# Optimization experiments

Hardware: AMD Instinct MI355X
Metric: run time of the kernel (lower is better)

The kernel has to match this reference:

```python
import jax, jax.numpy as jnp
import numpy as np

B, N, D_IN, D, H, L, NQ, NC, HID = 4, 25000, 32, 256, 8, 6, 100, 18, 1024


def _ln(x, g, b, eps=1e-5):
    m = jnp.mean(x, -1, keepdims=True)
    v = jnp.mean((x - m) ** 2, -1, keepdims=True)
    return (x - m) / jnp.sqrt(v + eps) * g + b


def _mha(q, kv, wqkv, bqkv, wo, bo, h):
    # q: (B, Lq, d), kv: (B, Lk, d); torch nn.MultiheadAttention math
    d = q.shape[-1]
    dh = d // h
    wq, wk, wv = jnp.split(wqkv, 3, axis=0)
    bq, bk, bv = jnp.split(bqkv, 3)
    Q = (q @ wq.T + bq).reshape(q.shape[0], q.shape[1], h, dh)
    K = (kv @ wk.T + bk).reshape(kv.shape[0], kv.shape[1], h, dh)
    V = (kv @ wv.T + bv).reshape(kv.shape[0], kv.shape[1], h, dh)
    s = jnp.einsum('bqhd,bkhd->bhqk', Q, K) / jnp.asarray(np.sqrt(dh), Q.dtype)
    a = jax.nn.softmax(s, axis=-1)
    o = jnp.einsum('bhqk,bkhd->bqhd', a, V).reshape(q.shape)
    return o @ wo.T + bo


def setup_inputs() -> dict:
    key = jax.random.key(0)
    ks = list(jax.random.split(key, 20))
    ki = iter(ks)

    def p(shape, s=0.02):
        return jax.random.normal(next(ki), shape, jnp.float32) * s

    inp = {
        'x': jax.random.normal(next(ki), (B * N, D_IN), jnp.float32),
        'batch_offsets': jnp.arange(B + 1, dtype=jnp.int32) * N,
        'ip_w': p((D, D_IN)), 'ip_b': jnp.zeros((D,), jnp.float32),
        'ip_ln_g': jnp.ones((D,), jnp.float32), 'ip_ln_b': jnp.zeros((D,), jnp.float32),
        'xm_w1': p((D, D_IN)), 'xm_b1': jnp.zeros((D,), jnp.float32),
        'xm_w2': p((D, D)), 'xm_b2': jnp.zeros((D,), jnp.float32),
        'query_embed': p((NQ, D), 1.0),
        'ca_wqkv': p((L, 3 * D, D)), 'ca_bqkv': jnp.zeros((L, 3 * D), jnp.float32),
        'ca_wo': p((L, D, D)), 'ca_bo': jnp.zeros((L, D), jnp.float32),
        'sa_wqkv': p((L, 3 * D, D)), 'sa_bqkv': jnp.zeros((L, 3 * D), jnp.float32),
        'sa_wo': p((L, D, D)), 'sa_bo': jnp.zeros((L, D), jnp.float32),
        'sa_ln_g': jnp.ones((L, D), jnp.float32), 'sa_ln_b': jnp.zeros((L, D), jnp.float32),
        'ffn_w1': p((L, HID, D)), 'ffn_b1': jnp.zeros((L, HID), jnp.float32),
        'ffn_w2': p((L, D, HID)), 'ffn_b2': jnp.zeros((L, D), jnp.float32),
        'ffn_ln_g': jnp.ones((L, D), jnp.float32), 'ffn_ln_b': jnp.zeros((L, D), jnp.float32),
        'out_ln_g': jnp.ones((D,), jnp.float32), 'out_ln_b': jnp.zeros((D,), jnp.float32),
        'cls_w1': p((D, D)), 'cls_b1': jnp.zeros((D,), jnp.float32),
        'cls_w2': p((NC + 1, D)), 'cls_b2': jnp.zeros((NC + 1,), jnp.float32),
    }
    return inp


def reference(x, batch_offsets, ip_w, ip_b, ip_ln_g, ip_ln_b, xm_w1, xm_b1, xm_w2, xm_b2,
              query_embed, ca_wqkv, ca_bqkv, ca_wo, ca_bo, sa_wqkv, sa_bqkv, sa_wo, sa_bo,
              sa_ln_g, sa_ln_b, ffn_w1, ffn_b1, ffn_w2, ffn_b2, ffn_ln_g, ffn_ln_b,
              out_ln_g, out_ln_b, cls_w1, cls_b1, cls_w2, cls_b2):
    b = batch_offsets.shape[0] - 1  # uniform segments -> batched attention
    n = x.shape[0] // b
    # input_proj: Linear -> LayerNorm -> ReLU
    inst = jax.nn.relu(_ln(x @ ip_w.T + ip_b, ip_ln_g, ip_ln_b)).reshape(b, n, -1)
    # x_mask: Linear -> ReLU -> Linear
    mask_feats = (jax.nn.relu(x @ xm_w1.T + xm_b1) @ xm_w2.T + xm_b2).reshape(b, n, -1)
    query = jnp.broadcast_to(query_embed, (b,) + query_embed.shape)
    for i in range(ca_wqkv.shape[0]):
        # CrossAttentionLayer: NOTE original discards dropout/norm results -> pure residual
        query = _mha(query, inst, ca_wqkv[i], ca_bqkv[i], ca_wo[i], ca_bo[i], H) + query
        # SelfAttentionLayer: residual + LayerNorm
        query = _ln(_mha(query, query, sa_wqkv[i], sa_bqkv[i], sa_wo[i], sa_bo[i], H) + query,
                    sa_ln_g[i], sa_ln_b[i])
        # FFN: residual + LayerNorm
        ff = jax.nn.relu(query @ ffn_w1[i].T + ffn_b1[i]) @ ffn_w2[i].T + ffn_b2[i]
        query = _ln(ff + query, ffn_ln_g[i], ffn_ln_b[i])
    qn = _ln(query, out_ln_g, out_ln_b)
    pred_labels = jax.nn.relu(qn @ cls_w1.T + cls_b1) @ cls_w2.T + cls_b2  # (b, NQ, NC+1)
    pred_masks = jnp.einsum('bqd,bnd->bqn', qn, mask_feats)  # (b, NQ, n)
    return pred_labels, pred_masks
```

## Files before the change

### kernel.cpp

```cpp
#include <hip/hip_runtime.h>

typedef unsigned short u16;
typedef unsigned int   u32;

constexpr int Bz   = 4;
constexpr int Ni   = 25000;
constexpr int BNi  = Bz * Ni;
constexpr int DIN  = 32;
constexpr int D    = 256;
constexpr int Hh   = 8;
constexpr int DH   = 32;
constexpr int Ll   = 6;
constexpr int NQ   = 100;
constexpr int NC1  = 19;
constexpr int HIDd = 1024;

constexpr int CHUNK  = 1250;
constexpr int NCHUNK = Ni / CHUNK;
constexpr size_t PARTB = (size_t)Hh * NCHUNK * 128 * 34;
constexpr float SM_SCALE = 0.17677669529663687f;

__device__ __forceinline__ u16 f2b(float f) {
    union { __bf16 h; u16 u; } c; c.h = (__bf16)f; return c.u;
}
__device__ __forceinline__ u32 pk2(float a, float b) {
    union { __bf16 h[2]; u32 u; } c; c.h[0] = (__bf16)a; c.h[1] = (__bf16)b; return c.u;
}

__global__ void k_cvt(const float* __restrict__ in, u16* __restrict__ out, int n) {
    for (int i = blockIdx.x * blockDim.x + threadIdx.x; i < n; i += gridDim.x * blockDim.x)
        out[i] = f2b(in[i]);
}

struct CvtJobs { const float* s[9]; u16* d[9]; int n[9]; };
__global__ __launch_bounds__(256) void k_cvtall(CvtJobs j) {
    const int job = blockIdx.y;
    const float* s = j.s[job];
    u16* d = j.d[job];
    const int n = j.n[job];
    for (int i = blockIdx.x * 256 + threadIdx.x; i < n; i += gridDim.x * 256)
        d[i] = f2b(s[i]);
}

__device__ __forceinline__ void gload16(const u16* g, u16* l) {
    __builtin_amdgcn_global_load_lds(
        (const __attribute__((address_space(1))) void*)g,
        (__attribute__((address_space(3))) void*)l, 16, 0, 0);
}

typedef __attribute__((ext_vector_type(8))) __bf16 bf8v;
typedef __attribute__((ext_vector_type(8))) short  s8v;
typedef __attribute__((ext_vector_type(4))) float  f4v;

template<bool DOLN>
__global__ __launch_bounds__(512) void k_inproj(
    const float* __restrict__ x, int row0, int Mloc,
    const u16* __restrict__ w16, const float* __restrict__ bias,
    const float* __restrict__ g, const float* __restrict__ bb,
    u16* __restrict__ outb)
{
    __shared__ u16 Ws[256 * 40];
    __shared__ float Cb[256], Cg[256], Cbb[256];
    const int tid = threadIdx.x, lane = tid & 63, w = tid >> 6;
    const int lr = lane & 15, hi = lane >> 4;

    for (int ch = tid; ch < 1024; ch += 512) {
        int r = ch >> 2, g4 = ch & 3;
        *(uint4*)&Ws[r * 40 + g4 * 8] = *(const uint4*)(w16 + r * 32 + g4 * 8);
    }
    if (tid < 256) {
        Cb[tid] = bias[tid];
        if (DOLN) { Cg[tid] = g[tid]; Cbb[tid] = bb[tid]; }
    }

    const int rloc = blockIdx.x * 128 + w * 16 + lr;
    const int gr = row0 + min(rloc, Mloc - 1);
    bf8v xf;
    {
        const float* xp = x + (size_t)gr * DIN + hi * 8;
        float4 a = *(const float4*)xp, c = *(const float4*)(xp + 4);
        union { s8v s; bf8v b; } u;
        u.s[0] = (short)f2b(a.x); u.s[1] = (short)f2b(a.y);
        u.s[2] = (short)f2b(a.z); u.s[3] = (short)f2b(a.w);
        u.s[4] = (short)f2b(c.x); u.s[5] = (short)f2b(c.y);
        u.s[6] = (short)f2b(c.z); u.s[7] = (short)f2b(c.w);
        xf = u.b;
    }
    __syncthreads();

    f4v acc[16];
    #pragma unroll
    for (int ci = 0; ci < 16; ci++) {
        acc[ci] = (f4v){0.f, 0.f, 0.f, 0.f};
        bf8v af = *(const bf8v*)&Ws[(ci * 16 + lr) * 40 + hi * 8];
        acc[ci] = __builtin_amdgcn_mfma_f32_16x16x32_bf16(af, xf, acc[ci], 0, 0, 0);
    }
    #pragma unroll
    for (int ci = 0; ci < 16; ci++)
        #pragma unroll
        for (int r = 0; r < 4; r++)
            acc[ci][r] += Cb[ci * 16 + hi * 4 + r];

    float mean = 0.f, ri = 1.f;
    if (DOLN) {
        float s = 0.f, q = 0.f;
        #pragma unroll
        for (int ci = 0; ci < 16; ci++)
            #pragma unroll
            for (int r = 0; r < 4; r++) { s += acc[ci][r]; q += acc[ci][r] * acc[ci][r]; }
        s += __shfl_xor(s, 16); s += __shfl_xor(s, 32);
        q += __shfl_xor(q, 16); q += __shfl_xor(q, 32);
        mean = s * (1.f / D);
        float var = q * (1.f / D) - mean * mean;
        ri = rsqrtf(var + 1e-5f);
    }
    if (rloc < Mloc) {
        #pragma unroll
        for (int ci = 0; ci < 16; ci++) {
            float v0[4];
            #pragma unroll
            for (int r = 0; r < 4; r++) {
                float v = acc[ci][r];
                if (DOLN) v = (v - mean) * ri * Cg[ci * 16 + hi * 4 + r] + Cbb[ci * 16 + hi * 4 + r];
                v0[r] = fmaxf(v, 0.f);
            }
            uint2 pkv;
            pkv.x = pk2(v0[0], v0[1]);
            pkv.y = pk2(v0[2], v0[3]);
            *(uint2*)&outb[(size_t)rloc * 256 + ci * 16 + hi * 4] = pkv;
        }
    }
}

__global__ __launch_bounds__(256) void k_ln(
    const float* __restrict__ in, float* __restrict__ out,
    const float* __restrict__ g, const float* __restrict__ b)
{
    const int t = threadIdx.x;
    const int row = blockIdx.x;
    float v = in[(size_t)row * D + t];
    float s = v, q = v * v;
    #pragma unroll
    for (int off = 32; off >= 1; off >>= 1) { s += __shfl_xor(s, off); q += __shfl_xor(q, off); }
    __shared__ float red[2][4];
    const int wid = t >> 6;
    if ((t & 63) == 0) { red[0][wid] = s; red[1][wid] = q; }
    __syncthreads();
    float S = red[0][0] + red[0][1] + red[0][2] + red[0][3];
    float Q = red[1][0] + red[1][1] + red[1][2] + red[1][3];
    float m   = S * (1.f / D);
    float var = Q * (1.f / D) - m * m;
    float ri  = rsqrtf(var + 1e-5f);
    out[(size_t)row * D + t] = (v - m) * ri * g[t] + b[t];
}

__global__ __launch_bounds__(256) void k_bcast(const float* __restrict__ qe, float* __restrict__ q)
{
    const int t = threadIdx.x;
    const int r = blockIdx.x;
    q[(size_t)r * D + t] = qe[(size_t)(r % NQ) * D + t];
}

template<int BM, int BN, int TM, int TN>
__global__ __launch_bounds__(256) void k_gemm(
    const float* __restrict__ A, const float* __restrict__ W,
    const float* __restrict__ bias, const float* __restrict__ resid,
    float* __restrict__ C, int M, int N, int K, int relu)
{
    constexpr int BK = 16;
    constexpr int TX = BN / TN, TY = BM / TM;
    static_assert(TX * TY == 256, "block must be 256 threads");
    __shared__ float As[BK][BM + 4];
    __shared__ float Ws[BK][BN + 4];

    const int tid = threadIdx.x;
    const int tx = tid % TX, ty = tid / TX;
    const int row0 = blockIdx.y * BM, col0 = blockIdx.x * BN;

    float acc[TM][TN];
    #pragma unroll
    for (int i = 0; i < TM; i++)
        #pragma unroll
        for (int j = 0; j < TN; j++) acc[i][j] = 0.f;

    for (int k0 = 0; k0 < K; k0 += BK) {
        __syncthreads();
        for (int idx = tid; idx < BM * (BK / 4); idx += 256) {
            int r = idx / (BK / 4), c4 = idx % (BK / 4);
            int gr = row0 + r;
            float4 v;
            if (gr < M) v = *(const float4*)(A + (size_t)gr * K + k0 + c4 * 4);
            else { v.x = v.y = v.z = v.w = 0.f; }
            As[c4*4+0][r] = v.x; As[c4*4+1][r] = v.y; As[c4*4+2][r] = v.z; As[c4*4+3][r] = v.w;
        }
        for (int idx = tid; idx < BN * (BK / 4); idx += 256) {
            int n = idx / (BK / 4), c4 = idx % (BK / 4);
            int gn = col0 + n;
            float4 v;
            if (gn < N) v = *(const float4*)(W + (size_t)gn * K + k0 + c4 * 4);
            else { v.x = v.y = v.z = v.w = 0.f; }
            Ws[c4*4+0][n] = v.x; Ws[c4*4+1][n] = v.y; Ws[c4*4+2][n] = v.z; Ws[c4*4+3][n] = v.w;
        }
        __syncthreads();
        #pragma unroll
        for (int kk = 0; kk < BK; kk++) {
            float a[TM], bb[TN];
            #pragma unroll
            for (int i = 0; i < TM; i++) a[i] = As[kk][ty * TM + i];
            #pragma unroll
            for (int j = 0; j < TN; j++) bb[j] = Ws[kk][tx * TN + j];
            #pragma unroll
            for (int i = 0; i < TM; i++)
                #pragma unroll
                for (int j = 0; j < TN; j++)
                    acc[i][j] = fmaf(a[i], bb[j], acc[i][j]);
        }
    }

    #pragma unroll
    for (int i = 0; i < TM; i++) {
        int gr = row0 + ty * TM + i;
        if (gr >= M) continue;
        #pragma unroll
        for (int j = 0; j < TN; j++) {
            int gn = col0 + tx * TN + j;
            if (gn >= N) continue;
            float v = acc[i][j];
            if (bias)  v += bias[gn];
            if (resid) v += resid[(size_t)gr * N + gn];
            if (relu)  v = fmaxf(v, 0.f);
            C[(size_t)gr * N + gn] = v;
        }
    }
}

template<bool RELU>
__global__ __launch_bounds__(256) void mm_small(
    const float* __restrict__ A, const u16* __restrict__ W,
    const float* __restrict__ bias, const float* __restrict__ resid,
    float* __restrict__ C, int M, int N, int K)
{
    __shared__ u16 As[64 * 40];
    __shared__ u16 Bs[64 * 40];
    const int tid  = threadIdx.x;
    const int lane = tid & 63, w = tid >> 6;
    const int wm = w >> 1, wn = w & 1;
    const int row0 = blockIdx.y * 64, col0 = blockIdx.x * 64;
    const int lr = lane & 15, hi = lane >> 4;

    f4v acc[2][2];
    #pragma unroll
    for (int i = 0; i < 2; i++)
        #pragma unroll
        for (int j = 0; j < 2; j++) acc[i][j] = (f4v){0.f, 0.f, 0.f, 0.f};

    const int sr = tid >> 2, sc = (tid & 3) * 8;
    const int ga = min(row0 + sr, M - 1);
    const int gw = min(col0 + sr, N - 1);

    for (int k0 = 0; k0 < K; k0 += 32) {
        __syncthreads();
        {
            const float* ap = A + (size_t)ga * K + k0 + sc;
            float4 a = *(const float4*)ap, c = *(const float4*)(ap + 4);
            uint4 u;
            u.x = pk2(a.x, a.y); u.y = pk2(a.z, a.w);
            u.z = pk2(c.x, c.y); u.w = pk2(c.z, c.w);
            *(uint4*)&As[sr * 40 + sc] = u;
            *(uint4*)&Bs[sr * 40 + sc] = *(const uint4*)(W + (size_t)gw * K + k0 + sc);
        }
        __syncthreads();
        bf8v a0 = *(const bf8v*)&As[(wm * 32      + lr) * 40 + hi * 8];
        bf8v a1 = *(const bf8v*)&As[(wm * 32 + 16 + lr) * 40 + hi * 8];
        bf8v b0 = *(const bf8v*)&Bs[(wn * 32      + lr) * 40 + hi * 8];
        bf8v b1 = *(const bf8v*)&Bs[(wn * 32 + 16 + lr) * 40 + hi * 8];
        acc[0][0] = __builtin_amdgcn_mfma_f32_16x16x32_bf16(a0, b0, acc[0][0], 0, 0, 0);
        acc[0][1] = __builtin_amdgcn_mfma_f32_16x16x32_bf16(a0, b1, acc[0][1], 0, 0, 0);
        acc[1][0] = __builtin_amdgcn_mfma_f32_16x16x32_bf16(a1, b0, acc[1][0], 0, 0, 0);
        acc[1][1] = __builtin_amdgcn_mfma_f32_16x16x32_bf16(a1, b1, acc[1][1], 0, 0, 0);
    }

    const int crl = hi * 4, ccl = lr;
    #pragma unroll
    for (int mi = 0; mi < 2; mi++)
        #pragma unroll
        for (int ni = 0; ni < 2; ni++)
            #pragma unroll
            for (int r = 0; r < 4; r++) {
                int grow = row0 + wm * 32 + mi * 16 + crl + r;
                int gcol = col0 + wn * 32 + ni * 16 + ccl;
                if (grow < M && gcol < N) {
                    float v = acc[mi][ni][r];
                    if (bias)  v += bias[gcol];
                    if (resid) v += resid[(size_t)grow * N + gcol];
                    if (RELU)  v = fmaxf(v, 0.f);
                    C[(size_t)grow * N + gcol] = v;
                }
            }
}

template<bool OUTBF>
__global__ __launch_bounds__(256) void mm128(
    const u16* __restrict__ A, const u16* __restrict__ W,
    const float* __restrict__ bias, void* __restrict__ Cv,
    int M, int N, int K, long long sA, long long sW, long long sC,
    int zmod, long long sW2, long long sBias)
{
    __shared__ u16 sm[8192];
    u16* As = sm;
    u16* Bs = sm + 4096;

    const int gx = gridDim.x, gy = gridDim.y;
    const int total = gx * gy * (int)gridDim.z;
    const int flat = blockIdx.x + gx * (blockIdx.y + gy * blockIdx.z);
    const int q8 = total >> 3, r8 = total & 7;
    const int xcd = flat & 7, blk = flat >> 3;
    const int swz = (xcd < r8 ? xcd * (q8 + 1) : r8 * (q8 + 1) + (xcd - r8) * q8) + blk;
    const int bx = swz % gx, by = (swz / gx) % gy, bz = swz / (gx * gy);

    const int aidx = bz % zmod, widx = bz / zmod;
    A += (size_t)aidx * sA;
    W += (size_t)aidx * sW + (size_t)widx * sW2;
    if (bias) bias += (size_t)widx * sBias;
    const int tid = threadIdx.x, lane = tid & 63, w = tid >> 6;
    const int wm = w >> 1, wn = w & 1;
    const int row0 = by * 128, col0 = bx * 128;
    const int lr = lane & 15, hi = lane >> 4;
    const int srow = lane >> 2, scol = (lane & 3) * 8;

    f4v acc[4][4];
    #pragma unroll
    for (int i = 0; i < 4; i++)
        #pragma unroll
        for (int j = 0; j < 4; j++) acc[i][j] = (f4v){0.f, 0.f, 0.f, 0.f};

    for (int k0 = 0; k0 < K; k0 += 32) {
        __syncthreads();
        #pragma unroll
        for (int i = 0; i < 2; i++) {
            const int c = w * 2 + i;
            const int row = c * 16 + srow;
            const int gra = min(row0 + row, M - 1);
            const int grb = min(col0 + row, N - 1);
            gload16(A + (size_t)gra * K + k0 + scol, &As[c * 512]);
            gload16(W + (size_t)grb * K + k0 + scol, &Bs[c * 512]);
        }
        __syncthreads();
        bf8v a[4], bb[4];
        #pragma unroll
        for (int mi = 0; mi < 4; mi++)
            a[mi] = *(const bf8v*)&As[(wm * 64 + mi * 16 + lr) * 32 + hi * 8];
        #pragma unroll
        for (int ni = 0; ni < 4; ni++)
            bb[ni] = *(const bf8v*)&Bs[(wn * 64 + ni * 16 + lr) * 32 + hi * 8];
        #pragma unroll
        for (int mi = 0; mi < 4; mi++)
            #pragma unroll
            for (int ni = 0; ni < 4; ni++)
                acc[mi][ni] = __builtin_amdgcn_mfma_f32_16x16x32_bf16(a[mi], bb[ni], acc[mi][ni], 0, 0, 0);
    }

    if (OUTBF) {
        #pragma unroll
        for (int h0 = 0; h0 < 2; h0++) {
            __syncthreads();
            if (wm == h0) {
                #pragma unroll
                for (int mi = 0; mi < 4; mi++)
                    #pragma unroll
                    for (int ni = 0; ni < 4; ni++) {
                        int gcol = col0 + wn * 64 + ni * 16 + lr;
                        float bv = bias ? bias[gcol] : 0.f;
                        #pragma unroll
                        for (int r = 0; r < 4; r++) {
                            int lrow = mi * 16 + hi * 4 + r;
                            sm[lrow * 128 + wn * 64 + ni * 16 + lr] = f2b(acc[mi][ni][r] + bv);
                        }
                    }
            }
            __syncthreads();
            u16* Cb16 = (u16*)Cv + (size_t)bz * sC;
            #pragma unroll
            for (int j = 0; j < 4; j++) {
                int idx = tid + j * 256;
                int lrow = idx >> 4, c16 = idx & 15;
                int grow = row0 + h0 * 64 + lrow;
                if (grow < M)
                    *(uint4*)(Cb16 + (size_t)grow * N + col0 + c16 * 8) =
                        *(const uint4*)&sm[lrow * 128 + c16 * 8];
            }
        }
    } else {
        const int crl = hi * 4, ccl = lr;
        float* Cf = (float*)Cv + (size_t)bz * sC;
        #pragma unroll
        for (int mi = 0; mi < 4; mi++)
            #pragma unroll
            for (int ni = 0; ni < 4; ni++)
                #pragma unroll
                for (int r = 0; r < 4; r++) {
                    int grow = row0 + wm * 64 + mi * 16 + crl + r;
                    int gcol = col0 + wn * 64 + ni * 16 + ccl;
                    if (grow < M && gcol < N) {
                        float v = acc[mi][ni][r];
                        if (bias) v += bias[gcol];
                        Cf[(size_t)grow * N + gcol] = v;
                    }
                }
    }
}

__global__ __launch_bounds__(512) void k_flash(
    const float* __restrict__ qbuf, const u16* __restrict__ kv,
    float* __restrict__ part, int bBase, size_t kvStride, size_t pStride)
{
    const int tid = threadIdx.x;
    const int lane = tid & 63, w = tid >> 6;
    const int h = blockIdx.y;
    const int b = bBase + blockIdx.z;
    const u16* kvp = kv + (size_t)blockIdx.z * kvStride;
    float* pp = part + (size_t)blockIdx.z * pStride;
    const int k0loc = blockIdx.x * CHUNK;
    const int lr = lane & 15, hi = lane >> 4;

    __shared__ u16 Ks[64 * 40];
    __shared__ u16 Vt[32 * 72];
    __shared__ u16 Pt[8][16 * 72];

    const int qt = w * 16 + lr;
    const int qg = b * NQ + min(qt, NQ - 1);
    bf8v qf;
    {
        const float* Qp = qbuf + (size_t)qg * D + h * DH + hi * 8;
        union { s8v s; bf8v b; } qu;
        #pragma unroll
        for (int j = 0; j < 8; j++) qu.s[j] = (short)f2b(Qp[j] * SM_SCALE);
        qf = qu.b;
    }

    float m = -1e30f, l = 0.f;
    f4v o0 = (f4v){0.f,0.f,0.f,0.f}, o1 = (f4v){0.f,0.f,0.f,0.f};

    constexpr int NSTEP = (CHUNK + 63) / 64;
    for (int s = 0; s < NSTEP; s++) {
        const int ck = k0loc + s * 64;
        const int nv = min(64, k0loc + CHUNK - ck);
        __syncthreads();
        if (tid < 256) {
            int key = tid >> 2, g = tid & 3;
            int krow = min(ck + key, Ni - 1);
            *(uint4*)&Ks[key * 40 + g * 8] =
                *(const uint4*)(kvp + (size_t)krow * (2 * D) + h * DH + g * 8);
        } else {
            int t2 = tid - 256;
            int key = t2 >> 2, g = t2 & 3;
            int krow = min(ck + key, Ni - 1);
            uint4 u = *(const uint4*)(kvp + (size_t)krow * (2 * D) + D + h * DH + g * 8);
            const u16* pu = (const u16*)&u;
            #pragma unroll
            for (int j = 0; j < 8; j++) Vt[(g * 8 + j) * 72 + key] = pu[j];
        }
        __syncthreads();

        f4v sf[4];
        #pragma unroll
        for (int j = 0; j < 4; j++) {
            bf8v kf = *(const bf8v*)&Ks[(j * 16 + lr) * 40 + hi * 8];
            sf[j] = (f4v){0.f,0.f,0.f,0.f};
            sf[j] = __builtin_amdgcn_mfma_f32_16x16x32_bf16(kf, qf, sf[j], 0, 0, 0);
        }

        float sv[16];
        #pragma unroll
        for (int j = 0; j < 4; j++)
            #pragma unroll
            for (int r = 0; r < 4; r++) {
                int key0 = j * 16 + hi * 4 + r;
                sv[j * 4 + r] = (key0 < nv) ? sf[j][r] : -1e30f;
            }
        float smax = sv[0];
        #pragma unroll
        for (int j = 1; j < 16; j++) smax = fmaxf(smax, sv[j]);
        smax = fmaxf(smax, __shfl_xor(smax, 16));
        smax = fmaxf(smax, __shfl_xor(smax, 32));
        float mnew  = fmaxf(m, smax);
        float scale = __expf(m - mnew);
        m = mnew;

        float pv[16];
        float psum = 0.f;
        #pragma unroll
        for (int j = 0; j < 16; j++) {
            pv[j] = __expf(sv[j] - mnew);
            psum += pv[j];
        }
        psum += __shfl_xor(psum, 16);
        psum += __shfl_xor(psum, 32);
        l = l * scale + psum;

        u16* pw = &Pt[w][lr * 72];
        #pragma unroll
        for (int j = 0; j < 4; j++) {
            *(u32*)&pw[j * 16 + hi * 4]     = pk2(pv[j*4+0], pv[j*4+1]);
            *(u32*)&pw[j * 16 + hi * 4 + 2] = pk2(pv[j*4+2], pv[j*4+3]);
        }

        const int qb4 = hi * 4;
        float f0 = __shfl(scale, qb4 + 0);
        float f1 = __shfl(scale, qb4 + 1);
        float f2 = __shfl(scale, qb4 + 2);
        float f3 = __shfl(scale, qb4 + 3);
        o0[0] *= f0; o0[1] *= f1; o0[2] *= f2; o0[3] *= f3;
        o1[0] *= f0; o1[1] *= f1; o1[2] *= f2; o1[3] *= f3;

        #pragma unroll
        for (int j = 0; j < 2; j++) {
            bf8v pf  = *(const bf8v*)&Pt[w][lr * 72 + j * 32 + hi * 8];
            bf8v vf0 = *(const bf8v*)&Vt[lr * 72 + j * 32 + hi * 8];
            bf8v vf1 = *(const bf8v*)&Vt[(16 + lr) * 72 + j * 32 + hi * 8];
            o0 = __builtin_amdgcn_mfma_f32_16x16x32_bf16(pf, vf0, o0, 0, 0, 0);
            o1 = __builtin_amdgcn_mfma_f32_16x16x32_bf16(pf, vf1, o1, 0, 0, 0);
        }
    }

    const size_t pbase = ((size_t)(h * NCHUNK + blockIdx.x) * 128) * 34;
    #pragma unroll
    for (int r = 0; r < 4; r++) {
        int qtr = w * 16 + hi * 4 + r;
        pp[pbase + (size_t)qtr * 34 + 2 + lr]      = o0[r];
        pp[pbase + (size_t)qtr * 34 + 2 + 16 + lr] = o1[r];
    }
    if (lane < 16) {
        pp[pbase + (size_t)(w * 16 + lane) * 34 + 0] = m;
        pp[pbase + (size_t)(w * 16 + lane) * 34 + 1] = l;
    }
}

__global__ __launch_bounds__(64) void k_fmerge(const float* __restrict__ part,
                                               float* __restrict__ abuf, int bBase, size_t pStride)
{
    const float* pz = part + (size_t)blockIdx.y * pStride;
    const int b = bBase + blockIdx.y;
    const int t = threadIdx.x;
    const int hq = blockIdx.x;
    const int h = hq / NQ, q = hq % NQ;
    float mmax = -1e30f;
    for (int c = 0; c < NCHUNK; c++)
        mmax = fmaxf(mmax, pz[((size_t)(h * NCHUNK + c) * 128 + q) * 34]);
    float L = 0.f, a = 0.f;
    for (int c = 0; c < NCHUNK; c++) {
        const float* p = &pz[((size_t)(h * NCHUNK + c) * 128 + q) * 34];
        float wv = __expf(p[0] - mmax);
        L += wv * p[1];
        if (t < DH) a += wv * p[2 + t];
    }
    if (t < DH)
        abuf[((size_t)(b * NQ + q)) * D + h * DH + t] = a / L;
}

__global__ __launch_bounds__(128) void k_sattn(const float* __restrict__ sqkv, float* __restrict__ abuf)
{
    const int tid = threadIdx.x;
    const int bh = blockIdx.x;
    const int b = bh >> 3, h = bh & 7;
    __shared__ float Ks[NQ][DH], Vs[NQ][DH];
    for (int idx = tid; idx < NQ * 8; idx += 128) {
        int kk = idx >> 3, f4 = idx & 7;
        const float* base = sqkv + ((size_t)(b * NQ + kk)) * (3 * D) + h * DH;
        *(float4*)&Ks[kk][f4 * 4] = *(const float4*)(base + D + f4 * 4);
        *(float4*)&Vs[kk][f4 * 4] = *(const float4*)(base + 2 * D + f4 * 4);
    }
    float qr[DH];
    const int q = tid;
    if (q < NQ) {
        const float* Qp = sqkv + ((size_t)(b * NQ + q)) * (3 * D) + h * DH;
        #pragma unroll
        for (int d = 0; d < DH; d += 4) {
            float4 v = *(const float4*)(Qp + d);
            qr[d] = v.x * SM_SCALE; qr[d+1] = v.y * SM_SCALE;
            qr[d+2] = v.z * SM_SCALE; qr[d+3] = v.w * SM_SCALE;
        }
    } else {
        #pragma unroll
        for (int d = 0; d < DH; d++) qr[d] = 0.f;
    }
    __syncthreads();
    float m = -1e30f, l = 0.f, acc[DH];
    #pragma unroll
    for (int d = 0; d < DH; d++) acc[d] = 0.f;
    for (int kk = 0; kk < NQ; kk++) {
        float sc = 0.f;
        #pragma unroll
        for (int d = 0; d < DH; d++) sc += qr[d] * Ks[kk][d];
        if (sc > m) {
            float r = __expf(m - sc);
            l *= r;
            #pragma unroll
            for (int d = 0; d < DH; d++) acc[d] *= r;
            m = sc;
        }
        float p = __expf(sc - m);
        l += p;
        #pragma unroll
        for (int d = 0; d < DH; d++) acc[d] += p * Vs[kk][d];
    }
    if (q < NQ) {
        float li = 1.f / l;
        float* o = abuf + ((size_t)(b * NQ + q)) * D + h * DH;
        #pragma unroll
        for (int d = 0; d < DH; d++) o[d] = acc[d] * li;
    }
}

extern "C" void kernel_launch(void* const* d_in, const int* in_sizes, int n_in,
                              void* d_out, int out_size, void* d_ws, size_t ws_size,
                              hipStream_t stream)
{
    const float* x        = (const float*)d_in[0];
    const float* ip_w     = (const float*)d_in[2];
    const float* ip_b     = (const float*)d_in[3];
    const float* ip_g     = (const float*)d_in[4];
    const float* ip_bb    = (const float*)d_in[5];
    const float* xm_w1    = (const float*)d_in[6];
    const float* xm_b1    = (const float*)d_in[7];
    const float* xm_w2    = (const float*)d_in[8];
    const float* xm_b2    = (const float*)d_in[9];
    const float* qe       = (const float*)d_in[10];
    const float* ca_wqkv  = (const float*)d_in[11];
    const float* ca_bqkv  = (const float*)d_in[12];
    const float* ca_wo    = (const float*)d_in[13];
    const float* ca_bo    = (const float*)d_in[14];
    const float* sa_wqkv  = (const float*)d_in[15];
    const float* sa_bqkv  = (const float*)d_in[16];
    const float* sa_wo    = (const float*)d_in[17];
    const float* sa_bo    = (const float*)d_in[18];
    const float* sa_ln_g  = (const float*)d_in[19];
    const float* sa_ln_b  = (const float*)d_in[20];
    const float* ffn_w1   = (const float*)d_in[21];
    const float* ffn_b1   = (const float*)d_in[22];
    const float* ffn_w2   = (const float*)d_in[23];
    const float* ffn_b2   = (const float*)d_in[24];
    const float* ffn_ln_g = (const float*)d_in[25];
    const float* ffn_ln_b = (const float*)d_in[26];
    const float* out_ln_g = (const float*)d_in[27];
    const float* out_ln_b = (const float*)d_in[28];
    const float* cls_w1   = (const float*)d_in[29];
    const float* cls_b1   = (const float*)d_in[30];
    const float* cls_w2   = (const float*)d_in[31];
    const float* cls_b2   = (const float*)d_in[32];
    float* out = (float*)d_out;

    bool batched = false;
    int kvG = 1;
    int instRows;
    if      (ws_size >= 740000000ull) { batched = true; kvG = 6; instRows = BNi; }
    else if (ws_size >= 430000000ull) { batched = true; kvG = 3; instRows = BNi; }
    else if (ws_size >= 210000000ull) { batched = true; kvG = 1; instRows = BNi; }
    else if (ws_size >= 112000000ull) { instRows = BNi; }
    else if (ws_size >=  73000000ull) { instRows = Ni;  }
    else return;
    const bool instFull = (instRows == BNi);
    const int nzb = batched ? Bz : 1;

    char* wp = (char*)d_ws;
    auto alloc = [&](size_t bytes) -> char* {
        char* r = wp; wp += (bytes + 255) & ~(size_t)255; return r;
    };
    u16*   instb = (u16*)  alloc((size_t)instRows * D * 2);
    u16*   kvb   = (u16*)  alloc((batched ? (size_t)kvG * Bz * Ni * 2 * D : (size_t)Ni * 2 * D) * 2);
    float* part  = (float*)alloc((size_t)nzb * PARTB * 4);
    float* qbuf  = (float*)alloc(409600);
    float* abuf  = (float*)alloc(409600);
    float* sqkv  = (float*)alloc(1228800);
    float* f1b   = (float*)alloc(1638400);
    float* qA    = (float*)alloc(409600);
    float* qB    = (float*)alloc(409600);
    u16*   ipw16 = (u16*)  alloc(256 * 32 * 2);
    u16*   xw116 = (u16*)  alloc(256 * 32 * 2);
    u16*   xw216 = (u16*)  alloc((size_t)D * D * 2);
    u16*   caq16 = (u16*)  alloc((size_t)Ll * 3 * D * D * 2);
    u16*   saq16 = (u16*)  alloc((size_t)Ll * 3 * D * D * 2);
    u16*   cao16 = (u16*)  alloc((size_t)Ll * D * D * 2);
    u16*   sao16 = (u16*)  alloc((size_t)Ll * D * D * 2);
    u16*   fw116 = (u16*)  alloc((size_t)Ll * HIDd * D * 2);
    u16*   fw216 = (u16*)  alloc((size_t)Ll * D * HIDd * 2);
    u16*   qnb   = (u16*)  alloc((size_t)Bz * NQ * D * 2);

    {
        CvtJobs j;
        j.s[0] = ip_w;    j.d[0] = ipw16; j.n[0] = 256 * 32;
        j.s[1] = xm_w1;   j.d[1] = xw116; j.n[1] = 256 * 32;
        j.s[2] = xm_w2;   j.d[2] = xw216; j.n[2] = D * D;
        j.s[3] = ca_wqkv; j.d[3] = caq16; j.n[3] = Ll * 3 * D * D;
        j.s[4] = sa_wqkv; j.d[4] = saq16; j.n[4] = Ll * 3 * D * D;
        j.s[5] = ca_wo;   j.d[5] = cao16; j.n[5] = Ll * D * D;
        j.s[6] = sa_wo;   j.d[6] = sao16; j.n[6] = Ll * D * D;
        j.s[7] = ffn_w1;  j.d[7] = fw116; j.n[7] = Ll * HIDd * D;
        j.s[8] = ffn_w2;  j.d[8] = fw216; j.n[8] = Ll * D * HIDd;
        k_cvtall<<<dim3(48, 9), 256, 0, stream>>>(j);
    }

    if (instFull)
        k_inproj<true><<<(BNi + 127) / 128, 512, 0, stream>>>(
            x, 0, BNi, ipw16, ip_b, ip_g, ip_bb, instb);
    k_bcast<<<Bz * NQ, 256, 0, stream>>>(qe, qA);

    float* qcur = qA;
    float* qtmp = qB;

    auto layer_tail = [&](int i) {
        mm_small<false><<<dim3(4, 7), 256, 0, stream>>>(
            abuf, cao16 + (size_t)i * D * D, ca_bo + (size_t)i * D, qcur, qtmp,
            Bz * NQ, D, D);
        { float* t2 = qcur; qcur = qtmp; qtmp = t2; }
        mm_small<false><<<dim3(12, 7), 256, 0, stream>>>(
            qcur, saq16 + (size_t)i * 3 * D * D, sa_bqkv + (size_t)i * 3 * D, nullptr, sqkv,
            Bz * NQ, 3 * D, D);
        k_sattn<<<Bz * Hh, 128, 0, stream>>>(sqkv, abuf);
        mm_small<false><<<dim3(4, 7), 256, 0, stream>>>(
            abuf, sao16 + (size_t)i * D * D, sa_bo + (size_t)i * D, qcur, qtmp,
            Bz * NQ, D, D);
        k_ln<<<Bz * NQ, 256, 0, stream>>>(qtmp, qtmp, sa_ln_g + i * D, sa_ln_b + i * D);
        { float* t2 = qcur; qcur = qtmp; qtmp = t2; }
        mm_small<true><<<dim3(16, 7), 256, 0, stream>>>(
            qcur, fw116 + (size_t)i * HIDd * D, ffn_b1 + (size_t)i * HIDd, nullptr, f1b,
            Bz * NQ, HIDd, D);
        mm_small<false><<<dim3(4, 7), 256, 0, stream>>>(
            f1b, fw216 + (size_t)i * D * HIDd, ffn_b2 + (size_t)i * D, qcur, qtmp,
            Bz * NQ, D, HIDd);
        k_ln<<<Bz * NQ, 256, 0, stream>>>(qtmp, qtmp, ffn_ln_g + i * D, ffn_ln_b + i * D);
        { float* t2 = qcur; qcur = qtmp; qtmp = t2; }
    };

    if (batched) {
        for (int l0 = 0; l0 < Ll; l0 += kvG) {
            mm128<true><<<dim3(4, 196, 4 * kvG), 256, 0, stream>>>(
                instb, caq16 + (size_t)l0 * 3 * D * D + (size_t)D * D,
                ca_bqkv + (size_t)l0 * 3 * D + D, kvb, Ni, 2 * D, D,
                (long long)Ni * D, 0, (long long)Ni * 2 * D,
                4, (long long)3 * D * D, (long long)3 * D);
            for (int i = l0; i < l0 + kvG; i++) {
                const u16* wq16 = caq16 + (size_t)i * 3 * D * D;
                const float* bqkv = ca_bqkv + (size_t)i * 3 * D;
                mm_small<false><<<dim3(4, 7), 256, 0, stream>>>(
                    qcur, wq16, bqkv, nullptr, qbuf, Bz * NQ, D, D);
                const u16* kvl = kvb + (size_t)(i - l0) * Bz * Ni * 2 * D;
                k_flash<<<dim3(NCHUNK, Hh, 4), 512, 0, stream>>>(
                    qbuf, kvl, part, 0, (size_t)Ni * 2 * D, PARTB);
                k_fmerge<<<dim3(Hh * NQ, 4), 64, 0, stream>>>(part, abuf, 0, PARTB);
                layer_tail(i);
            }
        }
    } else {
        for (int i = 0; i < Ll; i++) {
            const u16* wq16  = caq16 + (size_t)i * 3 * D * D;
            const u16* wkv16 = wq16 + (size_t)D * D;
            const float* bqkv = ca_bqkv + (size_t)i * 3 * D;
            mm_small<false><<<dim3(4, 7), 256, 0, stream>>>(
                qcur, wq16, bqkv, nullptr, qbuf, Bz * NQ, D, D);
            for (int b = 0; b < Bz; b++) {
                if (!instFull)
                    k_inproj<true><<<(Ni + 127) / 128, 512, 0, stream>>>(
                        x, b * Ni, Ni, ipw16, ip_b, ip_g, ip_bb, instb);
                const u16* ip = instFull ? instb + (size_t)b * Ni * D : instb;
                mm128<true><<<dim3(4, 196, 1), 256, 0, stream>>>(
                    ip, wkv16, bqkv + D, kvb, Ni, 2 * D, D, 0, 0, 0, 4, 0, 0);
                k_flash<<<dim3(NCHUNK, Hh, 1), 512, 0, stream>>>(
                    qbuf, kvb, part, b, 0, 0);
                k_fmerge<<<dim3(Hh * NQ, 1), 64, 0, stream>>>(part, abuf, b, 0);
            }
            layer_tail(i);
        }
    }

    float* qn = qbuf;
    k_ln<<<Bz * NQ, 256, 0, stream>>>(qcur, qn, out_ln_g, out_ln_b);
    k_gemm<64,64,4,4><<<dim3(4, 7), 256, 0, stream>>>(
        qn, cls_w1, cls_b1, nullptr, abuf, Bz * NQ, D, D, 1);
    k_gemm<64,64,4,4><<<dim3(1, 7), 256, 0, stream>>>(
        abuf, cls_w2, cls_b2, nullptr, out, Bz * NQ, NC1, D, 0);

    k_cvt<<<128, 256, 0, stream>>>(qn, qnb, Bz * NQ * D);
    if (instFull) {
        k_inproj<false><<<(BNi + 127) / 128, 512, 0, stream>>>(
            x, 0, BNi, xw116, xm_b1, nullptr, nullptr, instb);
        if (batched) {
            mm128<true><<<dim3(2, 196, 4), 256, 0, stream>>>(
                instb, xw216, xm_b2, kvb, Ni, D, D,
                (long long)Ni * D, 0, (long long)Ni * D, 4, 0, 0);
            mm128<false><<<dim3(196, 1, 4), 256, 0, stream>>>(
                qnb, kvb, nullptr, out + Bz * NQ * NC1, NQ, Ni, D,
                (long long)NQ * D, (long long)Ni * D, (long long)NQ * Ni, 4, 0, 0);
        } else {
            for (int b = 0; b < Bz; b++) {
                mm128<true><<<dim3(2, 196, 1), 256, 0, stream>>>(
                    instb + (size_t)b * Ni * D, xw216, xm_b2, kvb, Ni, D, D, 0, 0, 0, 4, 0, 0);
                mm128<false><<<dim3(196, 1, 1), 256, 0, stream>>>(
                    qnb + (size_t)b * NQ * D, kvb, nullptr,
                    out + Bz * NQ * NC1 + (size_t)b * NQ * Ni, NQ, Ni, D, 0, 0, 0, 4, 0, 0);
            }
        }
    } else {
        for (int b = 0; b < Bz; b++) {
            k_inproj<false><<<(Ni + 127) / 128, 512, 0, stream>>>(
                x, b * Ni, Ni, xw116, xm_b1, nullptr, nullptr, instb);
            mm128<true><<<dim3(2, 196, 1), 256, 0, stream>>>(
                instb, xw216, xm_b2, kvb, Ni, D, D, 0, 0, 0, 4, 0, 0);
            mm128<false><<<dim3(196, 1, 1), 256, 0, stream>>>(
                qnb + (size_t)b * NQ * D, kvb, nullptr,
                out + Bz * NQ * NC1 + (size_t)b * NQ * Ni, NQ, Ni, D, 0, 0, 0, 4, 0, 0);
        }
    }
}
```

Measured before the change: 1.710 ms.

## Fuse cross-attention K/V projection into flash attention kernel

The separate K/V projection GEMM, which wrote a large bf16 KV buffer, is removed. Each flash-attention block now loads its head's K and V weight slices into shared memory and computes the K/V tiles for 32 keys at a time from the inst activations. The block index is remapped so neighbouring blocks, likely sharing an XCD, work on the same batch and chunk. This cuts HBM traffic for the KV write and read but recomputes the projection per head, halves the key step, and drops the workspace-size fallback paths.

Result: slower. 1.960 ms (+14.6%).

```diff
diff --git a/kernel.cpp b/kernel.cpp
--- a/kernel.cpp
+++ b/kernel.cpp
@@ -17,6 +17,8 @@
 
 constexpr int CHUNK  = 1250;
 constexpr int NCHUNK = Ni / CHUNK;
+constexpr int KSTEP  = 32;
+constexpr int NSTEP  = (CHUNK + KSTEP - 1) / KSTEP;
 constexpr size_t PARTB = (size_t)Hh * NCHUNK * 128 * 34;
 constexpr float SM_SCALE = 0.17677669529663687f;
 
@@ -410,69 +412,110 @@
     }
 }
 
-__global__ __launch_bounds__(512) void k_flash(
-    const float* __restrict__ qbuf, const u16* __restrict__ kv,
-    float* __restrict__ part, int bBase, size_t kvStride, size_t pStride)
-{
-    const int tid = threadIdx.x;
-    const int lane = tid & 63, w = tid >> 6;
-    const int h = blockIdx.y;
-    const int b = bBase + blockIdx.z;
-    const u16* kvp = kv + (size_t)blockIdx.z * kvStride;
-    float* pp = part + (size_t)blockIdx.z * pStride;
-    const int k0loc = blockIdx.x * CHUNK;
+__global__ __launch_bounds__(512) void k_fused(
+    const float* __restrict__ qbuf, const u16* __restrict__ instb,
+    const u16* __restrict__ wk,
+    const float* __restrict__ bkv,
+    float* __restrict__ part)
+{
+    __shared__ u16 Wks[32 * 264];
+    __shared__ u16 Wvs[32 * 264];
+    __shared__ u16 instT[32 * 264];
+    __shared__ u16 Ks[32 * 40];
+    __shared__ u16 Vt[32 * 40];
+    u16* Pt = instT;
+
+    const int f = blockIdx.x + NCHUNK * (blockIdx.y + Hh * (int)blockIdx.z);
+    const int xcd = f & 7, slot = f >> 3;
+    const int g = xcd * 10 + (slot >> 3);
+    const int h = slot & 7;
+    const int c = g % NCHUNK, b = g / NCHUNK;
+
+    const int tid = threadIdx.x, lane = tid & 63, w = tid >> 6;
     const int lr = lane & 15, hi = lane >> 4;
-
-    __shared__ u16 Ks[64 * 40];
-    __shared__ u16 Vt[32 * 72];
-    __shared__ u16 Pt[8][16 * 72];
+    const int k0loc = c * CHUNK;
+    const u16* instB = instb + (size_t)b * Ni * D;
+    const u16* wkh = wk + (size_t)(h * DH) * D;
+    const u16* wvh = wk + (size_t)D * D + (size_t)(h * DH) * D;
+
+    for (int idx = tid; idx < 2048; idx += 512) {
+        int which = idx >> 10;
+        int r = (idx >> 5) & 31, c8 = idx & 31;
+        const u16* src = (which ? wvh : wkh) + (size_t)r * D + c8 * 8;
+        u16* dst = (which ? Wvs : Wks) + r * 264 + c8 * 8;
+        *(uint4*)dst = *(const uint4*)src;
+    }
 
     const int qt = w * 16 + lr;
     const int qg = b * NQ + min(qt, NQ - 1);
     bf8v qf;
     {
         const float* Qp = qbuf + (size_t)qg * D + h * DH + hi * 8;
-        union { s8v s; bf8v b; } qu;
+        union { s8v s; bf8v b2; } qu;
         #pragma unroll
         for (int j = 0; j < 8; j++) qu.s[j] = (short)f2b(Qp[j] * SM_SCALE);
-        qf = qu.b;
+        qf = qu.b2;
+    }
+
+    const int isV = w >> 2;
+    const int w2 = w & 3;
+    const int ktw = w2 & 1, dtw = w2 >> 1;
+    float kb = 0.f, vb[4];
+    if (!isV) {
+        kb = bkv[h * DH + dtw * 16 + lr];
+    } else {
+        #pragma unroll
+        for (int r = 0; r < 4; r++) vb[r] = bkv[D + h * DH + dtw * 16 + hi * 4 + r];
     }
 
     float m = -1e30f, l = 0.f;
     f4v o0 = (f4v){0.f,0.f,0.f,0.f}, o1 = (f4v){0.f,0.f,0.f,0.f};
 
-    constexpr int NSTEP = (CHUNK + 63) / 64;
     for (int s = 0; s < NSTEP; s++) {
-        const int ck = k0loc + s * 64;
-        const int nv = min(64, k0loc + CHUNK - ck);
-        __syncthreads();
-        if (tid < 256) {
-            int key = tid >> 2, g = tid & 3;
-            int krow = min(ck + key, Ni - 1);
-            *(uint4*)&Ks[key * 40 + g * 8] =
-                *(const uint4*)(kvp + (size_t)krow * (2 * D) + h * DH + g * 8);
+        const int ck = k0loc + s * KSTEP;
+        const int nv = min(KSTEP, k0loc + CHUNK - ck);
+        __syncthreads();
+        for (int idx = tid; idx < 1024; idx += 512) {
+            int r = idx >> 5, c8 = idx & 31;
+            int grow = min(ck + r, Ni - 1);
+            *(uint4*)&instT[r * 264 + c8 * 8] =
+                *(const uint4*)(instB + (size_t)grow * D + c8 * 8);
+        }
+        __syncthreads();
+        f4v pacc = (f4v){0.f,0.f,0.f,0.f};
+        #pragma unroll
+        for (int kk = 0; kk < 8; kk++) {
+            bf8v af, bf;
+            if (!isV) {
+                af = *(const bf8v*)&instT[(ktw * 16 + lr) * 264 + kk * 32 + hi * 8];
+                bf = *(const bf8v*)&Wks[(dtw * 16 + lr) * 264 + kk * 32 + hi * 8];
+            } else {
+                af = *(const bf8v*)&Wvs[(dtw * 16 + lr) * 264 + kk * 32 + hi * 8];
+                bf = *(const bf8v*)&instT[(ktw * 16 + lr) * 264 + kk * 32 + hi * 8];
+            }
+            pacc = __builtin_amdgcn_mfma_f32_16x16x32_bf16(af, bf, pacc, 0, 0, 0);
+        }
+        if (!isV) {
+            #pragma unroll
+            for (int r = 0; r < 4; r++)
+                Ks[(ktw * 16 + hi * 4 + r) * 40 + dtw * 16 + lr] = f2b(pacc[r] + kb);
         } else {
-            int t2 = tid - 256;
-            int key = t2 >> 2, g = t2 & 3;
-            int krow = min(ck + key, Ni - 1);
-            uint4 u = *(const uint4*)(kvp + (size_t)krow * (2 * D) + D + h * DH + g * 8);
-            const u16* pu = (const u16*)&u;
-            #pragma unroll
-            for (int j = 0; j < 8; j++) Vt[(g * 8 + j) * 72 + key] = pu[j];
-        }
-        __syncthreads();
-
-        f4v sf[4];
-        #pragma unroll
-        for (int j = 0; j < 4; j++) {
+            #pragma unroll
+            for (int r = 0; r < 4; r++)
+                Vt[(dtw * 16 + hi * 4 + r) * 40 + ktw * 16 + lr] = f2b(pacc[r] + vb[r]);
+        }
+        __syncthreads();
+
+        f4v sf[2];
+        #pragma unroll
+        for (int j = 0; j < 2; j++) {
             bf8v kf = *(const bf8v*)&Ks[(j * 16 + lr) * 40 + hi * 8];
             sf[j] = (f4v){0.f,0.f,0.f,0.f};
             sf[j] = __builtin_amdgcn_mfma_f32_16x16x32_bf16(kf, qf, sf[j], 0, 0, 0);
         }
-
-        float sv[16];
-        #pragma unroll
-        for (int j = 0; j < 4; j++)
+        float sv[8];
+        #pragma unroll
+        for (int j = 0; j < 2; j++)
             #pragma unroll
             for (int r = 0; r < 4; r++) {
                 int key0 = j * 16 + hi * 4 + r;
@@ -480,27 +523,24 @@
             }
         float smax = sv[0];
         #pragma unroll
-        for (int j = 1; j < 16; j++) smax = fmaxf(smax, sv[j]);
+        for (int j = 1; j < 8; j++) smax = fmaxf(smax, sv[j]);
         smax = fmaxf(smax, __shfl_xor(smax, 16));
         smax = fmaxf(smax, __shfl_xor(smax, 32));
         float mnew  = fmaxf(m, smax);
         float scale = __expf(m - mnew);
         m = mnew;
 
-        float pv[16];
+        float pv[8];
         float psum = 0.f;
         #pragma unroll
-        for (int j = 0; j < 16; j++) {
-            pv[j] = __expf(sv[j] - mnew);
-            psum += pv[j];
-        }
+        for (int j = 0; j < 8; j++) { pv[j] = __expf(sv[j] - mnew); psum += pv[j]; }
         psum += __shfl_xor(psum, 16);
         psum += __shfl_xor(psum, 32);
         l = l * scale + psum;
 
-        u16* pw = &Pt[w][lr * 72];
-        #pragma unroll
-        for (int j = 0; j < 4; j++) {
+        u16* pw = &Pt[(size_t)w * 640 + lr * 40];
+        #pragma unroll
+        for (int j = 0; j < 2; j++) {
             *(u32*)&pw[j * 16 + hi * 4]     = pk2(pv[j*4+0], pv[j*4+1]);
             *(u32*)&pw[j * 16 + hi * 4 + 2] = pk2(pv[j*4+2], pv[j*4+3]);
         }
@@ -513,17 +553,15 @@
         o0[0] *= f0; o0[1] *= f1; o0[2] *= f2; o0[3] *= f3;
         o1[0] *= f0; o1[1] *= f1; o1[2] *= f2; o1[3] *= f3;
 
-        #pragma unroll
-        for (int j = 0; j < 2; j++) {
-            bf8v pf  = *(const bf8v*)&Pt[w][lr * 72 + j * 32 + hi * 8];
-            bf8v vf0 = *(const bf8v*)&Vt[lr * 72 + j * 32 + hi * 8];
-            bf8v vf1 = *(const bf8v*)&Vt[(16 + lr) * 72 + j * 32 + hi * 8];
-            o0 = __builtin_amdgcn_mfma_f32_16x16x32_bf16(pf, vf0, o0, 0, 0, 0);
-            o1 = __builtin_amdgcn_mfma_f32_16x16x32_bf16(pf, vf1, o1, 0, 0, 0);
-        }
-    }
-
-    const size_t pbase = ((size_t)(h * NCHUNK + blockIdx.x) * 128) * 34;
+        bf8v pf  = *(const bf8v*)&Pt[(size_t)w * 640 + lr * 40 + hi * 8];
+        bf8v vf0 = *(const bf8v*)&Vt[lr * 40 + hi * 8];
+        bf8v vf1 = *(const bf8v*)&Vt[(16 + lr) * 40 + hi * 8];
+        o0 = __builtin_amdgcn_mfma_f32_16x16x32_bf16(pf, vf0, o0, 0, 0, 0);
+        o1 = __builtin_amdgcn_mfma_f32_16x16x32_bf16(pf, vf1, o1, 0, 0, 0);
+    }
+
+    float* pp = part + (size_t)b * PARTB;
+    const size_t pbase = ((size_t)(h * NCHUNK + c) * 128) * 34;
     #pragma unroll
     for (int r = 0; r < 4; r++) {
         int qtr = w * 16 + hi * 4 + r;
@@ -650,25 +688,15 @@
     const float* cls_b2   = (const float*)d_in[32];
     float* out = (float*)d_out;
 
-    bool batched = false;
-    int kvG = 1;
-    int instRows;
-    if      (ws_size >= 740000000ull) { batched = true; kvG = 6; instRows = BNi; }
-    else if (ws_size >= 430000000ull) { batched = true; kvG = 3; instRows = BNi; }
-    else if (ws_size >= 210000000ull) { batched = true; kvG = 1; instRows = BNi; }
-    else if (ws_size >= 112000000ull) { instRows = BNi; }
-    else if (ws_size >=  73000000ull) { instRows = Ni;  }
-    else return;
-    const bool instFull = (instRows == BNi);
-    const int nzb = batched ? Bz : 1;
+    if (ws_size < 160000000ull) return;
 
     char* wp = (char*)d_ws;
     auto alloc = [&](size_t bytes) -> char* {
         char* r = wp; wp += (bytes + 255) & ~(size_t)255; return r;
     };
-    u16*   instb = (u16*)  alloc((size_t)instRows * D * 2);
-    u16*   kvb   = (u16*)  alloc((batched ? (size_t)kvG * Bz * Ni * 2 * D : (size_t)Ni * 2 * D) * 2);
-    float* part  = (float*)alloc((size_t)nzb * PARTB * 4);
+    u16*   instb = (u16*)  alloc((size_t)BNi * D * 2);
+    u16*   kvb   = (u16*)  alloc((size_t)Bz * Ni * D * 2);
+    float* part  = (float*)alloc((size_t)Bz * PARTB * 4);
     float* qbuf  = (float*)alloc(409600);
     float* abuf  = (float*)alloc(409600);
     float* sqkv  = (float*)alloc(1228800);
@@ -700,15 +728,21 @@
         k_cvtall<<<dim3(48, 9), 256, 0, stream>>>(j);
     }
 
-    if (instFull)
-        k_inproj<true><<<(BNi + 127) / 128, 512, 0, stream>>>(
-            x, 0, BNi, ipw16, ip_b, ip_g, ip_bb, instb);
+    k_inproj<true><<<(BNi + 127) / 128, 512, 0, stream>>>(
+        x, 0, BNi, ipw16, ip_b, ip_g, ip_bb, instb);
     k_bcast<<<Bz * NQ, 256, 0, stream>>>(qe, qA);
 
     float* qcur = qA;
     float* qtmp = qB;
 
-    auto layer_tail = [&](int i) {
+    for (int i = 0; i < Ll; i++) {
+        const u16*   wq16 = caq16 + (size_t)i * 3 * D * D;
+        const float* bqkv = ca_bqkv + (size_t)i * 3 * D;
+        mm_small<false><<<dim3(4, 7), 256, 0, stream>>>(
+            qcur, wq16, bqkv, nullptr, qbuf, Bz * NQ, D, D);
+        k_fused<<<dim3(NCHUNK, Hh, Bz), 512, 0, stream>>>(
+            qbuf, instb, wq16 + (size_t)D * D, bqkv + D, part);
+        k_fmerge<<<dim3(Hh * NQ, Bz), 64, 0, stream>>>(part, abuf, 0, PARTB);
         mm_small<false><<<dim3(4, 7), 256, 0, stream>>>(
             abuf, cao16 + (size_t)i * D * D, ca_bo + (size_t)i * D, qcur, qtmp,
             Bz * NQ, D, D);
@@ -730,47 +764,6 @@
             Bz * NQ, D, HIDd);
         k_ln<<<Bz * NQ, 256, 0, stream>>>(qtmp, qtmp, ffn_ln_g + i * D, ffn_ln_b + i * D);
         { float* t2 = qcur; qcur = qtmp; qtmp = t2; }
-    };
-
-    if (batched) {
-        for (int l0 = 0; l0 < Ll; l0 += kvG) {
-            mm128<true><<<dim3(4, 196, 4 * kvG), 256, 0, stream>>>(
-                instb, caq16 + (size_t)l0 * 3 * D * D + (size_t)D * D,
-                ca_bqkv + (size_t)l0 * 3 * D + D, kvb, Ni, 2 * D, D,
-                (long long)Ni * D, 0, (long long)Ni * 2 * D,
-                4, (long long)3 * D * D, (long long)3 * D);
-            for (int i = l0; i < l0 + kvG; i++) {
-                const u16* wq16 = caq16 + (size_t)i * 3 * D * D;
-                const float* bqkv = ca_bqkv + (size_t)i * 3 * D;
-                mm_small<false><<<dim3(4, 7), 256, 0, stream>>>(
-                    qcur, wq16, bqkv, nullptr, qbuf, Bz * NQ, D, D);
-                const u16* kvl = kvb + (size_t)(i - l0) * Bz * Ni * 2 * D;
-                k_flash<<<dim3(NCHUNK, Hh, 4), 512, 0, stream>>>(
-                    qbuf, kvl, part, 0, (size_t)Ni * 2 * D, PARTB);
-                k_fmerge<<<dim3(Hh * NQ, 4), 64, 0, stream>>>(part, abuf, 0, PARTB);
-                layer_tail(i);
-            }
-        }
-    } else {
-        for (int i = 0; i < Ll; i++) {
-            const u16* wq16  = caq16 + (size_t)i * 3 * D * D;
-            const u16* wkv16 = wq16 + (size_t)D * D;
-            const float* bqkv = ca_bqkv + (size_t)i * 3 * D;
-            mm_small<false><<<dim3(4, 7), 256, 0, stream>>>(
-                qcur, wq16, bqkv, nullptr, qbuf, Bz * NQ, D, D);
-            for (int b = 0; b < Bz; b++) {
-                if (!instFull)
-                    k_inproj<true><<<(Ni + 127) / 128, 512, 0, stream>>>(
-                        x, b * Ni, Ni, ipw16, ip_b, ip_g, ip_bb, instb);
-                const u16* ip = instFull ? instb + (size_t)b * Ni * D : instb;
-                mm128<true><<<dim3(4, 196, 1), 256, 0, stream>>>(
-                    ip, wkv16, bqkv + D, kvb, Ni, 2 * D, D, 0, 0, 0, 4, 0, 0);
-                k_flash<<<dim3(NCHUNK, Hh, 1), 512, 0, stream>>>(
-                    qbuf, kvb, part, b, 0, 0);
-                k_fmerge<<<dim3(Hh * NQ, 1), 64, 0, stream>>>(part, abuf, b, 0);
-            }
-            layer_tail(i);
-        }
     }
 
     float* qn = qbuf;
@@ -781,34 +774,12 @@
         abuf, cls_w2, cls_b2, nullptr, out, Bz * NQ, NC1, D, 0);
 
     k_cvt<<<128, 256, 0, stream>>>(qn, qnb, Bz * NQ * D);
-    if (instFull) {
-        k_inproj<false><<<(BNi + 127) / 128, 512, 0, stream>>>(
-            x, 0, BNi, xw116, xm_b1, nullptr, nullptr, instb);
-        if (batched) {
-            mm128<true><<<dim3(2, 196, 4), 256, 0, stream>>>(
-                instb, xw216, xm_b2, kvb, Ni, D, D,
-                (long long)Ni * D, 0, (long long)Ni * D, 4, 0, 0);
-            mm128<false><<<dim3(196, 1, 4), 256, 0, stream>>>(
-                qnb, kvb, nullptr, out + Bz * NQ * NC1, NQ, Ni, D,
-                (long long)NQ * D, (long long)Ni * D, (long long)NQ * Ni, 4, 0, 0);
-        } else {
-            for (int b = 0; b < Bz; b++) {
-                mm128<true><<<dim3(2, 196, 1), 256, 0, stream>>>(
-                    instb + (size_t)b * Ni * D, xw216, xm_b2, kvb, Ni, D, D, 0, 0, 0, 4, 0, 0);
-                mm128<false><<<dim3(196, 1, 1), 256, 0, stream>>>(
-                    qnb + (size_t)b * NQ * D, kvb, nullptr,
-                    out + Bz * NQ * NC1 + (size_t)b * NQ * Ni, NQ, Ni, D, 0, 0, 0, 4, 0, 0);
-            }
-        }
-    } else {
-        for (int b = 0; b < Bz; b++) {
-            k_inproj<false><<<(Ni + 127) / 128, 512, 0, stream>>>(
-                x, b * Ni, Ni, xw116, xm_b1, nullptr, nullptr, instb);
-            mm128<true><<<dim3(2, 196, 1), 256, 0, stream>>>(
-                instb, xw216, xm_b2, kvb, Ni, D, D, 0, 0, 0, 4, 0, 0);
-            mm128<false><<<dim3(196, 1, 1), 256, 0, stream>>>(
-                qnb + (size_t)b * NQ * D, kvb, nullptr,
-                out + Bz * NQ * NC1 + (size_t)b * NQ * Ni, NQ, Ni, D, 0, 0, 0, 4, 0, 0);
-        }
-    }
-}
+    k_inproj<false><<<(BNi + 127) / 128, 512, 0, stream>>>(
+        x, 0, BNi, xw116, xm_b1, nullptr, nullptr, instb);
+    mm128<true><<<dim3(2, 196, 4), 256, 0, stream>>>(
+        instb, xw216, xm_b2, kvb, Ni, D, D,
+        (long long)Ni * D, 0, (long long)Ni * D, 4, 0, 0);
+    mm128<false><<<dim3(196, 1, 4), 256, 0, stream>>>(
+        qnb, kvb, nullptr, out + Bz * NQ * NC1, NQ, Ni, D,
+        (long long)NQ * D, (long long)Ni * D, (long long)NQ * Ni, 4, 0, 0);
+}
```
